# Optimization experiments

Measured on AMD Instinct MI355X. Metric: run time of the kernel, lower is better.

The kernel has to match this reference:

```python
import jax, jax.numpy as jnp
import numpy as np

TEMPERATURE = 0.07
BASE_TEMPERATURE = 0.07
EPS = 0.0001  # matches the +0.0001 in the torch code


def _l2norm(x):
    return x / jnp.clip(jnp.linalg.norm(x, axis=-1, keepdims=True), 1e-12, None)


def setup_inputs() -> dict:
    key = jax.random.key(0)
    k1, k2, k3 = jax.random.split(key, 3)
    # Sampled hard anchors: [total_classes=102, n_view=10, d=256], unit-norm
    # (original normalizes feats with F.normalize before _hard_anchor_sampling).
    X_anchor = _l2norm(jax.random.normal(k1, (102, 10, 256), dtype=jnp.float32))
    y_anchor = jax.random.randint(k2, (102,), 0, 19)
    # Memory queue of negatives: [class_num=19, cache_size=5000, d=256], unit-norm.
    queue = _l2norm(jax.random.normal(k3, (19, 5000, 256), dtype=jnp.float32))
    return {"X_anchor": X_anchor, "y_anchor": y_anchor, "queue": queue}


def reference(X_anchor, y_anchor, queue):
    anchor_num, n_view, d = X_anchor.shape
    class_num, cache_size, _ = queue.shape

    # anchor_feature = cat(unbind(X_anchor, dim=1), dim=0)  -> view-major order [n_view*anchor_num, d]
    anchor_feature = jnp.transpose(X_anchor, (1, 0, 2)).reshape(n_view * anchor_num, d)
    # _sample_negative flattens the queue class-major: [class_num*cache_size, d]
    contrast_feature = queue.reshape(class_num * cache_size, d)

    # mask = eq(y_anchor, y_contrast.T) then .repeat(anchor_count=n_view, contrast_count=1)
    y_a = jnp.tile(y_anchor, n_view)                                  # [N]
    y_c = jnp.repeat(jnp.arange(class_num, dtype=y_anchor.dtype), cache_size)  # [M]
    mask = (y_a[:, None] == y_c[None, :]).astype(X_anchor.dtype)      # [N, M]

    logits = jnp.matmul(anchor_feature, contrast_feature.T) / TEMPERATURE  # [N, M]
    logits_max = jax.lax.stop_gradient(jnp.max(logits, axis=1, keepdims=True))
    logits = logits - logits_max

    exp_logits = jnp.exp(logits)
    neg_sum = jnp.sum(exp_logits * (1.0 - mask), axis=1, keepdims=True)  # [N, 1]
    log_prob = logits - jnp.log(exp_logits + neg_sum)

    mean_log_prob_pos = jnp.sum(mask * log_prob, axis=1) / (jnp.sum(mask, axis=1) + EPS)
    loss = -(TEMPERATURE / BASE_TEMPERATURE) * mean_log_prob_pos
    return jnp.mean(loss)
```

## Files before the change

kernel.cpp:

```cpp
#include <hip/hip_runtime.h>
#include <hip/hip_bf16.h>
#include <stdint.h>

#define NCLS   19
#define CACHE  5000
#define NTILE  313
#define DDIM   256
#define NANCH  102
#define NVIEW  10
#define NROWS  1020
#define NSUB   13
#define NCHUNK (NCLS*NSUB)
#define NWG    (4*NCHUNK)
#define SCALE_A 20.6099319733f
#define LN2     0.69314718056f

using bf16x8 = __attribute__((ext_vector_type(8))) __bf16;
using f32x4  = __attribute__((ext_vector_type(4))) float;
using u16x8  = __attribute__((ext_vector_type(8))) unsigned short;

#if __has_builtin(__builtin_amdgcn_exp2f)
#define EXP2(x) __builtin_amdgcn_exp2f(x)
#else
#define EXP2(x) __expf((x) * LN2)
#endif

static __device__ __forceinline__ unsigned short f2bf(float x) {
    unsigned int u = __float_as_uint(x);
    unsigned int r = (u + 0x7FFFu + ((u >> 16) & 1u)) >> 16;
    return (unsigned short)r;
}

typedef const __attribute__((address_space(1))) void* gas_t;
typedef __attribute__((address_space(3))) void* las_t;

static __device__ __forceinline__ void stage16(const unsigned short* g, unsigned short* lw) {
    __builtin_amdgcn_global_load_lds((gas_t)(uintptr_t)g, (las_t)(uintptr_t)lw, 16, 0, 0);
}

__global__ __launch_bounds__(256) void conv_queue2(const float* __restrict__ Qf,
                                                   unsigned short* __restrict__ Qbf) {
    int i = blockIdx.x * 256 + threadIdx.x;
    int lane = i & 63;
    int kk   = (i >> 6) & 7;
    int tile = i >> 9;
    int cls  = tile / NTILE;
    int t    = tile - cls * NTILE;
    int lm = lane & 15, lg = lane >> 4;
    int cic = t * 16 + lm;
    int k   = kk * 32 + lg * 8;
    u16x8 o;
    if (cic < CACHE) {
        const float* src = Qf + ((size_t)cls * CACHE + cic) * DDIM + k;
        float4 v0 = *reinterpret_cast<const float4*>(src);
        float4 v1 = *reinterpret_cast<const float4*>(src + 4);
        o[0]=f2bf(v0.x); o[1]=f2bf(v0.y); o[2]=f2bf(v0.z); o[3]=f2bf(v0.w);
        o[4]=f2bf(v1.x); o[5]=f2bf(v1.y); o[6]=f2bf(v1.z); o[7]=f2bf(v1.w);
    } else {
        for (int q = 0; q < 8; ++q) o[q] = 0;
    }
    *reinterpret_cast<u16x8*>(Qbf + (size_t)i * 8) = o;
}

__global__ __launch_bounds__(256) void conv_anchor2(const float* __restrict__ X,
                                                    unsigned short* __restrict__ Abf) {
    int n = blockIdx.x;
    int k = threadIdx.x;
    float v = 0.f;
    if (n < NROWS) {
        int vv = n / NANCH, a = n - vv * NANCH;
        v = X[((size_t)a * NVIEW + vv) * DDIM + k] * SCALE_A;
    }
    Abf[(size_t)n * DDIM + k] = f2bf(v);
}

__global__ __launch_bounds__(256, 2) void pass1_kernel(
    const unsigned short* __restrict__ Abf, const unsigned short* __restrict__ Qbf,
    const int* __restrict__ y,
    float* __restrict__ Pt, float* __restrict__ Pe, float* __restrict__ Ps)
{
    __shared__ unsigned short lds[2][4096];

    int orig = blockIdx.x;
    int xcd = orig & 7, slot = orig >> 3;
    int wid = (xcd < 4 ? xcd * 124 : 496 + (xcd - 4) * 123) + slot;
    int rt = wid & 3;
    int cs = wid >> 2;
    int cls = cs / NSUB;
    int sub = cs - cls * NSUB;
    int t0 = (NTILE * sub) / NSUB, t1 = (NTILE * (sub + 1)) / NSUB;

    int tid = threadIdx.x;
    int wave = tid >> 6, lane = tid & 63;
    int lg = lane >> 4, lm = lane & 15;
    int wrb = rt * 256 + wave * 64;

    bf16x8 afrag[4][8];
    #pragma unroll
    for (int f = 0; f < 4; ++f)
        #pragma unroll
        for (int kk = 0; kk < 8; ++kk)
            afrag[f][kk] = *reinterpret_cast<const bf16x8*>(
                Abf + (size_t)(wrb + f * 16 + lm) * DDIM + kk * 32 + lg * 8);

    float mpos[4][4];
    int   rowidx[4][4];
    #pragma unroll
    for (int f = 0; f < 4; ++f)
        #pragma unroll
        for (int r = 0; r < 4; ++r) {
            int row = wrb + f * 16 + lg * 4 + r;
            rowidx[f][r] = row;
            mpos[f][r] = (row < NROWS && y[row % NANCH] == cls) ? 1.0f : 0.0f;
        }

    float tacc[4][4] = {}, sacc[4][4] = {};

    const unsigned short* qcls = Qbf + (size_t)cls * NTILE * 4096;

#define STAGE(buf, t) do {                                                        \
        stage16(qcls + (size_t)(t) * 4096 + tid * 8,        &lds[buf][wave * 512]);        \
        stage16(qcls + (size_t)(t) * 4096 + 2048 + tid * 8, &lds[buf][2048 + wave * 512]); \
    } while (0)

    STAGE(0, t0);
    __syncthreads();

    int nt = t1 - t0;
    for (int it = 0; it < nt; ++it) {
        int cur = it & 1;
        if (it + 1 < nt) STAGE(cur ^ 1, t0 + it + 1);

        bf16x8 bfrag[8];
        const unsigned short* lp = &lds[cur][lane * 8];
        #pragma unroll
        for (int kk = 0; kk < 8; ++kk)
            bfrag[kk] = *reinterpret_cast<const bf16x8*>(lp + kk * 512);

        f32x4 acc[4];
        #pragma unroll
        for (int f = 0; f < 4; ++f) acc[f] = (f32x4){0.f, 0.f, 0.f, 0.f};
        #pragma unroll
        for (int kk = 0; kk < 8; ++kk)
            #pragma unroll
            for (int f = 0; f < 4; ++f)
                acc[f] = __builtin_amdgcn_mfma_f32_16x16x32_bf16(afrag[f][kk], bfrag[kk], acc[f], 0, 0, 0);

        #pragma unroll
        for (int f = 0; f < 4; ++f)
            #pragma unroll
            for (int r = 0; r < 4; ++r) {
                float v = acc[f][r];
                tacc[f][r] += EXP2(v);
                sacc[f][r] += v;
            }
        __syncthreads();
    }
#undef STAGE

    #pragma unroll
    for (int f = 0; f < 4; ++f)
        #pragma unroll
        for (int r = 0; r < 4; ++r) {
            float t = tacc[f][r], s = sacc[f][r];
            #pragma unroll
            for (int m = 1; m < 16; m <<= 1) {
                t += __shfl_xor(t, m);
                s += __shfl_xor(s, m);
            }
            if (lm == 0) {
                size_t idx = (size_t)cs * 1024 + rowidx[f][r];
                float mp = mpos[f][r];
                Pt[idx] = t; Pe[idx] = mp * t; Ps[idx] = mp * s;
            }
        }
}

__global__ __launch_bounds__(256) void reduce_rows(const float* __restrict__ Pt,
                                                   const float* __restrict__ Pe,
                                                   const float* __restrict__ Ps,
                                                   float* __restrict__ rowloss) {
    int tid = threadIdx.x;
    int row = blockIdx.x * 64 + (tid >> 2);
    int part = tid & 3;
    float tot = 0.f, pe = 0.f, ps = 0.f;
    for (int c = part; c < NCHUNK; c += 4) {
        size_t idx = (size_t)c * 1024 + row;
        tot += Pt[idx]; pe += Pe[idx]; ps += Ps[idx];
    }
    tot += __shfl_xor(tot, 1); pe += __shfl_xor(pe, 1); ps += __shfl_xor(ps, 1);
    tot += __shfl_xor(tot, 2); pe += __shfl_xor(pe, 2); ps += __shfl_xor(ps, 2);
    if (part == 0) {
        float r = 0.f;
        if (row < NROWS) {
            float ns    = tot - pe - 144.0f;
            float pos_e = pe - 8.0f;
            float pos_s = ps * LN2;
            float sum_logprob = pos_s - (5000.0f * logf(ns) + pos_e / ns);
            r = -sum_logprob / (5000.0f + 1e-4f);
        }
        rowloss[row] = r;
    }
}

__global__ __launch_bounds__(256) void pass3_kernel(const float* __restrict__ rowloss,
                                                    float* __restrict__ out) {
    float local = 0.f;
    for (int n = threadIdx.x; n < 1024; n += 256) local += rowloss[n];
    #pragma unroll
    for (int m = 1; m < 64; m <<= 1) local += __shfl_xor(local, m);
    __shared__ float sb[4];
    if ((threadIdx.x & 63) == 0) sb[threadIdx.x >> 6] = local;
    __syncthreads();
    if (threadIdx.x == 0)
        out[0] = (sb[0] + sb[1] + sb[2] + sb[3]) * (1.0f / (float)NROWS);
}

extern "C" void kernel_launch(void* const* d_in, const int* in_sizes, int n_in,
                              void* d_out, int out_size, void* d_ws, size_t ws_size,
                              hipStream_t stream) {
    const float* X  = (const float*)d_in[0];
    const int*   y  = (const int*)d_in[1];
    const float* Qf = (const float*)d_in[2];
    float* out = (float*)d_out;

    char* ws = (char*)d_ws;
    unsigned short* Qbf = (unsigned short*)(ws);
    unsigned short* Abf = (unsigned short*)(ws + 48717824);
    float* Pt      = (float*)(ws + 49242112);
    float* Pe      = (float*)(ws + 50253824);
    float* Ps      = (float*)(ws + 51265536);
    float* rowloss = (float*)(ws + 52277248);

    conv_queue2<<<11894, 256, 0, stream>>>(Qf, Qbf);
    conv_anchor2<<<1024, 256, 0, stream>>>(X, Abf);
    pass1_kernel<<<NWG, 256, 0, stream>>>(Abf, Qbf, y, Pt, Pe, Ps);
    reduce_rows<<<16, 256, 0, stream>>>(Pt, Pe, Ps, rowloss);
    pass3_kernel<<<1, 256, 0, stream>>>(rowloss, out);
}
```

Measured before the change: 111.8 us.

## Load queue B-fragments directly into registers instead of staging through LDS

Drops the LDS double buffer filled with global_load_lds, along with its per-tile __syncthreads. Each wave now loads its own B fragments straight from global memory into two register buffers and ping-pongs between them. The per-row mask and row index setup moves into the epilogue, which lowers register pressure during the main loop. The trade-off is that each of the four waves now fetches the same tile itself instead of sharing one LDS copy, so global and L2 traffic rises about fourfold, and the extra B registers may hurt occupancy.

Result: no change. 112.9 us (+1.0%).

```diff
diff --git a/kernel.cpp b/kernel.cpp
--- a/kernel.cpp
+++ b/kernel.cpp
@@ -29,13 +29,6 @@
     unsigned int u = __float_as_uint(x);
     unsigned int r = (u + 0x7FFFu + ((u >> 16) & 1u)) >> 16;
     return (unsigned short)r;
-}
-
-typedef const __attribute__((address_space(1))) void* gas_t;
-typedef __attribute__((address_space(3))) void* las_t;
-
-static __device__ __forceinline__ void stage16(const unsigned short* g, unsigned short* lw) {
-    __builtin_amdgcn_global_load_lds((gas_t)(uintptr_t)g, (las_t)(uintptr_t)lw, 16, 0, 0);
 }
 
 __global__ __launch_bounds__(256) void conv_queue2(const float* __restrict__ Qf,
@@ -79,8 +72,6 @@
     const int* __restrict__ y,
     float* __restrict__ Pt, float* __restrict__ Pe, float* __restrict__ Ps)
 {
-    __shared__ unsigned short lds[2][4096];
-
     int orig = blockIdx.x;
     int xcd = orig & 7, slot = orig >> 3;
     int wid = (xcd < 4 ? xcd * 124 : 496 + (xcd - 4) * 123) + slot;
@@ -103,60 +94,50 @@
             afrag[f][kk] = *reinterpret_cast<const bf16x8*>(
                 Abf + (size_t)(wrb + f * 16 + lm) * DDIM + kk * 32 + lg * 8);
 
-    float mpos[4][4];
-    int   rowidx[4][4];
-    #pragma unroll
-    for (int f = 0; f < 4; ++f)
-        #pragma unroll
-        for (int r = 0; r < 4; ++r) {
-            int row = wrb + f * 16 + lg * 4 + r;
-            rowidx[f][r] = row;
-            mpos[f][r] = (row < NROWS && y[row % NANCH] == cls) ? 1.0f : 0.0f;
-        }
-
     float tacc[4][4] = {}, sacc[4][4] = {};
 
-    const unsigned short* qcls = Qbf + (size_t)cls * NTILE * 4096;
-
-#define STAGE(buf, t) do {                                                        \
-        stage16(qcls + (size_t)(t) * 4096 + tid * 8,        &lds[buf][wave * 512]);        \
-        stage16(qcls + (size_t)(t) * 4096 + 2048 + tid * 8, &lds[buf][2048 + wave * 512]); \
+    const bf16x8* qchunk = reinterpret_cast<const bf16x8*>(Qbf) + (size_t)cls * NTILE * 512 + lane;
+
+#define LOADB(dst, t) do {                                                    \
+        const bf16x8* _p = qchunk + (size_t)(t) * 512;                        \
+        _Pragma("unroll")                                                     \
+        for (int kk = 0; kk < 8; ++kk) dst[kk] = _p[kk * 64];                 \
     } while (0)
 
-    STAGE(0, t0);
-    __syncthreads();
-
+#define COMPUTE(bf) do {                                                      \
+        f32x4 acc[4];                                                         \
+        _Pragma("unroll")                                                     \
+        for (int f = 0; f < 4; ++f) acc[f] = (f32x4){0.f, 0.f, 0.f, 0.f};     \
+        _Pragma("unroll")                                                     \
+        for (int kk = 0; kk < 8; ++kk)                                        \
+            _Pragma("unroll")                                                 \
+            for (int f = 0; f < 4; ++f)                                       \
+                acc[f] = __builtin_amdgcn_mfma_f32_16x16x32_bf16(             \
+                    afrag[f][kk], bf[kk], acc[f], 0, 0, 0);                   \
+        _Pragma("unroll")                                                     \
+        for (int f = 0; f < 4; ++f)                                           \
+            _Pragma("unroll")                                                 \
+            for (int r = 0; r < 4; ++r) {                                     \
+                float v = acc[f][r];                         \
+                tacc[f][r] += EXP2(v);              \
+                sacc[f][r] += v;                                              \
+            }                                                                 \
+    } while (0)
+
+    bf16x8 bA[8], bB[8];
     int nt = t1 - t0;
-    for (int it = 0; it < nt; ++it) {
-        int cur = it & 1;
-        if (it + 1 < nt) STAGE(cur ^ 1, t0 + it + 1);
-
-        bf16x8 bfrag[8];
-        const unsigned short* lp = &lds[cur][lane * 8];
-        #pragma unroll
-        for (int kk = 0; kk < 8; ++kk)
-            bfrag[kk] = *reinterpret_cast<const bf16x8*>(lp + kk * 512);
-
-        f32x4 acc[4];
-        #pragma unroll
-        for (int f = 0; f < 4; ++f) acc[f] = (f32x4){0.f, 0.f, 0.f, 0.f};
-        #pragma unroll
-        for (int kk = 0; kk < 8; ++kk)
-            #pragma unroll
-            for (int f = 0; f < 4; ++f)
-                acc[f] = __builtin_amdgcn_mfma_f32_16x16x32_bf16(afrag[f][kk], bfrag[kk], acc[f], 0, 0, 0);
-
-        #pragma unroll
-        for (int f = 0; f < 4; ++f)
-            #pragma unroll
-            for (int r = 0; r < 4; ++r) {
-                float v = acc[f][r];
-                tacc[f][r] += EXP2(v);
-                sacc[f][r] += v;
-            }
-        __syncthreads();
-    }
-#undef STAGE
+    int it = 0;
+    LOADB(bA, t0);
+    for (;;) {
+        if (it + 1 < nt) LOADB(bB, t0 + it + 1);
+        COMPUTE(bA);
+        ++it; if (it == nt) break;
+        if (it + 1 < nt) LOADB(bA, t0 + it + 1);
+        COMPUTE(bB);
+        ++it; if (it == nt) break;
+    }
+#undef LOADB
+#undef COMPUTE
 
     #pragma unroll
     for (int f = 0; f < 4; ++f)
@@ -169,8 +150,9 @@
                 s += __shfl_xor(s, m);
             }
             if (lm == 0) {
-                size_t idx = (size_t)cs * 1024 + rowidx[f][r];
-                float mp = mpos[f][r];
+                int row = wrb + f * 16 + lg * 4 + r;
+                float mp = (row < NROWS && y[row % NANCH] == cls) ? 1.0f : 0.0f;
+                size_t idx = (size_t)cs * 1024 + row;
                 Pt[idx] = t; Pe[idx] = mp * t; Ps[idx] = mp * s;
             }
         }
```
